# Performance work log

Measured on AMD Instinct MI355X. Metric: run time of the kernel, lower is better.

## Reference

```python
import jax, jax.numpy as jnp
import numpy as np

# irreps = 128x0e + 64x1e + 32x2e  (dim = 128 + 64*3 + 32*5 = 480)
# hidden = 512x0e + 256x1e + 128x2e ; gate scalars = (256+128) x0e
N = 65536
M0, M1, M2 = 128, 64, 32          # input multiplicities per degree l=0,1,2
H0, H1, H2 = 512, 256, 128        # hidden multiplicities
G = H1 + H2                       # number of sigmoid gate scalars
EPS = 1e-8
S0 = float(np.sqrt(M0)); S1 = float(np.sqrt(M1)); S2 = float(np.sqrt(M2))
T0 = float(np.sqrt(H0)); T1 = float(np.sqrt(H1)); T2 = float(np.sqrt(H2))


def setup_inputs() -> dict:
    key = jax.random.key(0)
    ks = jax.random.split(key, 8)
    p = lambda k, shape: jax.random.normal(k, shape, dtype=jnp.float32)
    return dict(
        x=p(ks[0], (N, M0 + 3 * M1 + 5 * M2)),
        # SeperableLayerNorm affine params (weight per channel; bias only for scalars)
        nw0=jnp.ones((M0,), jnp.float32), nb0=jnp.zeros((M0,), jnp.float32),
        nw1=jnp.ones((M1,), jnp.float32), nw2=jnp.ones((M2,), jnp.float32),
        # lin1: irreps -> (hidden scalars + gates) 0e, hidden 1e, hidden 2e. e3nn fan-in norm.
        W0=p(ks[1], (M0, H0 + G)), b0=jnp.zeros((H0 + G,), jnp.float32),
        W1=p(ks[2], (M1, H1)), W2=p(ks[3], (M2, H2)),
        # lin2: gated hidden -> irreps
        V0=p(ks[4], (H0, M0)), c0=jnp.zeros((M0,), jnp.float32),
        V1=p(ks[5], (H1, M1)), V2=p(ks[6], (H2, M2)),
        alpha=jnp.float32(0.5),
    )


def _ffn(x, nw0, nb0, nw1, nw2, W0, b0, W1, W2, V0, c0, V1, V2, alpha):
    n = x.shape[0]
    x0 = x[:, :M0]                                   # [n, 128] scalars
    x1 = x[:, M0:M0 + 3 * M1].reshape(n, M1, 3)      # [n, 64, 3]
    x2 = x[:, M0 + 3 * M1:].reshape(n, M2, 5)        # [n, 32, 5]

    # --- SeperableLayerNorm (component norm, std_balance_degrees) ---
    # scalars: standard layer norm over scalar channels
    mu = jnp.mean(x0, axis=-1, keepdims=True)
    xc = x0 - mu
    y0 = xc * jax.lax.rsqrt(jnp.mean(xc * xc, axis=-1, keepdims=True) + EPS) * nw0 + nb0
    # l>0: RMS norm, each degree contributes equally (balance over degrees)
    s1 = jnp.mean(x1 * x1, axis=(1, 2))
    s2 = jnp.mean(x2 * x2, axis=(1, 2))
    inv = jax.lax.rsqrt(0.5 * (s1 + s2) + EPS)[:, None, None]
    y1 = x1 * inv * nw1[:, None]
    y2 = x2 * inv * nw2[:, None]

    # --- lin1 (e3nn Linear: per-degree block matmul, 1/sqrt(fan_in), bias on 0e) ---
    h0 = y0 @ W0 / S0 + b0                            # [n, 896]
    h1 = jnp.einsum('num,uw->nwm', y1, W1) / S1       # [n, 256, 3]
    h2 = jnp.einsum('num,uw->nwm', y2, W2) / S2       # [n, 128, 5]

    # --- Gate: silu on hidden scalars, sigmoid gates broadcast onto l>0 ---
    s = jax.nn.silu(h0[:, :H0])
    g = jax.nn.sigmoid(h0[:, H0:])
    z1 = h1 * g[:, :H1, None]
    z2 = h2 * g[:, H1:, None]

    # --- lin2 ---
    o0 = s @ V0 / T0 + c0
    o1 = jnp.einsum('num,uw->nwm', z1, V1) / T1
    o2 = jnp.einsum('num,uw->nwm', z2, V2) / T2
    dx = jnp.concatenate([o0, o1.reshape(n, -1), o2.reshape(n, -1)], axis=-1)
    return x + jnp.tanh(alpha) * dx


def reference(x, nw0, nb0, nw1, nw2, W0, b0, W1, W2, V0, c0, V1, V2, alpha):
    return _ffn(x, nw0, nb0, nw1, nw2, W0, b0, W1, W2, V0, c0, V1, V2, alpha)
```

## Files before the change

kernel.cpp:

```cpp
#include <hip/hip_runtime.h>
#include <stdint.h>

#define NROWS 65536
#define DCOL  480
#define RT    16

#define INV_S0 0.08838834764831845f
#define INV_S1 0.125f
#define INV_S2 0.17677669529663687f
#define INV_T0 0.044194173824159216f
#define INV_T1 0.0625f
#define INV_T2 0.08838834764831845f

#define OFF_W0T 0
#define OFF_W1T 114688
#define OFF_W2T 131072
#define OFF_V0T 135168
#define OFF_V1T 200704
#define OFF_V2T 217088
#define TOT_W   221184

typedef __attribute__((ext_vector_type(8))) short  short8;
typedef __attribute__((ext_vector_type(4))) float  floatx4;

__device__ __forceinline__ uint16_t f2bf(float x){
  uint32_t u = __builtin_bit_cast(uint32_t, x);
  return (uint16_t)((u + 0x8000u) >> 16);
}
__device__ __forceinline__ float bf2f(uint16_t h){
  return __builtin_bit_cast(float, (uint32_t)h << 16);
}

#define MFMA16(a,b,c) __builtin_amdgcn_mfma_f32_16x16x32_bf16((a),(b),(c),0,0,0)

__global__ __launch_bounds__(256)
void convert_weights(const float* __restrict__ W0, const float* __restrict__ W1,
                     const float* __restrict__ W2, const float* __restrict__ V0,
                     const float* __restrict__ V1, const float* __restrict__ V2,
                     uint16_t* __restrict__ wt)
{
  const int tid = blockIdx.x*256 + threadIdx.x;
  if (tid >= TOT_W) return;
  if (tid < OFF_W1T){
    const int i = tid;            const int n = i>>7, k = i&127;
    wt[tid] = f2bf(W0[(size_t)k*896 + n] * INV_S0);
  } else if (tid < OFF_W2T){
    const int i = tid - OFF_W1T;  const int n = i>>6, k = i&63;
    wt[tid] = f2bf(W1[(size_t)k*256 + n] * INV_S1);
  } else if (tid < OFF_V0T){
    const int i = tid - OFF_W2T;  const int n = i>>5, k = i&31;
    wt[tid] = f2bf(W2[(size_t)k*128 + n] * INV_S2);
  } else if (tid < OFF_V1T){
    const int i = tid - OFF_V0T;  const int n = i>>9, k = i&511;
    wt[tid] = f2bf(V0[(size_t)k*128 + n] * INV_T0);
  } else if (tid < OFF_V2T){
    const int i = tid - OFF_V1T;  const int n = i>>8, k = i&255;
    wt[tid] = f2bf(V1[(size_t)k*64 + n] * INV_T1);
  } else {
    const int i = tid - OFF_V2T;  const int n = i>>7, k = i&127;
    wt[tid] = f2bf(V2[(size_t)k*32 + n] * INV_T2);
  }
}

__global__ __launch_bounds__(256, 3)
void ffn_mfma(const float* __restrict__ x,  const float* __restrict__ nw0,
              const float* __restrict__ nb0,const float* __restrict__ nw1,
              const float* __restrict__ nw2,const float* __restrict__ b0,
              const float* __restrict__ c0, const float* __restrict__ alpha,
              const uint16_t* __restrict__ wt, float* __restrict__ out)
{
  __shared__ __align__(16) uint16_t y0bf[16][136];
  __shared__ __align__(16) uint16_t y1bf[3][16][72];
  __shared__ __align__(16) uint16_t y2bf[5][16][40];
  __shared__ __align__(16) uint16_t gbf[16][392];
  __shared__ __align__(16) uint16_t sbf[16][520];

  const int t      = threadIdx.x;
  const int wave   = t >> 6, lane = t & 63;
  const int lane16 = lane & 15, quad = lane >> 4;
  const int row0   = blockIdx.x * RT;
  const float ta   = tanhf(alpha[0]);

  {
    for (int rr = 0; rr < 4; ++rr){
      const int r = wave*4 + rr;
      const float* xr = x + (size_t)(row0 + r)*DCOL;
      float xv[8];
      #pragma unroll
      for (int i=0;i<8;++i){ const int e = lane + i*64; xv[i] = (e < DCOL) ? xr[e] : 0.f; }
      float s0  = xv[0] + xv[1];
      float s0q = xv[0]*xv[0] + xv[1]*xv[1];
      float q1  = xv[2]*xv[2] + xv[3]*xv[3] + xv[4]*xv[4];
      float q2  = xv[5]*xv[5] + xv[6]*xv[6] + xv[7]*xv[7];
      #pragma unroll
      for (int off=32; off>0; off>>=1){
        s0  += __shfl_xor(s0,  off);
        s0q += __shfl_xor(s0q, off);
        q1  += __shfl_xor(q1,  off);
        q2  += __shfl_xor(q2,  off);
      }
      const float mu   = s0 * (1.f/128.f);
      const float var  = s0q * (1.f/128.f) - mu*mu;
      const float rstd = rsqrtf(var + 1e-8f);
      const float inv  = rsqrtf(0.5f*(q1*(1.f/192.f) + q2*(1.f/160.f)) + 1e-8f);
      #pragma unroll
      for (int i=0;i<8;++i){
        const int e = lane + i*64;
        if (e < 128){
          y0bf[r][e] = f2bf((xv[i]-mu)*rstd*nw0[e] + nb0[e]);
        } else if (e < 320){
          const int d = e - 128; const int u = d/3, mm = d - 3*u;
          y1bf[mm][r][u] = f2bf(xv[i]*inv*nw1[u]);
        } else if (e < DCOL){
          const int d = e - 320; const int u = d/5, mm = d - 5*u;
          y2bf[mm][r][u] = f2bf(xv[i]*inv*nw2[u]);
        }
      }
    }
  }
  __syncthreads();

  {
    short8 a0[4];
    #pragma unroll
    for (int kk=0; kk<4; ++kk)
      a0[kk] = *(const short8*)&y0bf[lane16][kk*32 + quad*8];
    const uint16_t* W0t = wt + OFF_W0T;
    #pragma unroll 1
    for (int tile = wave; tile < 56; tile += 4){
      const int n0 = tile*16;
      floatx4 acc = {0.f,0.f,0.f,0.f};
      #pragma unroll
      for (int kk=0; kk<4; ++kk){
        const short8 b = *(const short8*)(W0t + (size_t)(n0+lane16)*128 + kk*32 + quad*8);
        acc = MFMA16(a0[kk], b, acc);
      }
      const int col  = n0 + lane16;
      const float bias = b0[col];
      #pragma unroll
      for (int r2=0; r2<4; ++r2){
        const int row = quad*4 + r2;
        const float h  = acc[r2] + bias;
        const float sg = 1.f/(1.f + __expf(-h));
        if (col < 512) sbf[row][col]       = f2bf(h*sg);
        else           gbf[row][col - 512] = f2bf(sg);
      }
    }
  }
  __syncthreads();

  {
    const uint16_t* V0t = wt + OFF_V0T;
    const int n0a = wave*16, n0b = (wave+4)*16;
    floatx4 acc0 = {0.f,0.f,0.f,0.f}, acc1 = {0.f,0.f,0.f,0.f};
    #pragma unroll 2
    for (int kk=0; kk<16; ++kk){
      const short8 a  = *(const short8*)&sbf[lane16][kk*32 + quad*8];
      const short8 ba = *(const short8*)(V0t + (size_t)(n0a+lane16)*512 + kk*32 + quad*8);
      const short8 bb = *(const short8*)(V0t + (size_t)(n0b+lane16)*512 + kk*32 + quad*8);
      acc0 = MFMA16(a, ba, acc0);
      acc1 = MFMA16(a, bb, acc1);
    }
    #pragma unroll
    for (int tt=0; tt<2; ++tt){
      const int col = (tt ? n0b : n0a) + lane16;
      const float cc = c0[col];
      const floatx4 acc = tt ? acc1 : acc0;
      #pragma unroll
      for (int r2=0; r2<4; ++r2){
        const int row = quad*4 + r2;
        const size_t idx = (size_t)(row0+row)*DCOL + col;
        out[idx] = x[idx] + ta*(acc[r2] + cc);
      }
    }
  }
  __syncthreads();

  uint16_t (*zbf1)[264] = (uint16_t (*)[264])&sbf[0][0];
  uint16_t (*zbf2)[136] = (uint16_t (*)[136])&sbf[0][0];

  {
    const uint16_t* W1t = wt + OFF_W1T;
    const uint16_t* V1t = wt + OFF_V1T;
    #pragma unroll 1
    for (int m=0; m<3; ++m){
      {
        const short8 a0 = *(const short8*)&y1bf[m][lane16][quad*8];
        const short8 a1 = *(const short8*)&y1bf[m][lane16][32 + quad*8];
        #pragma unroll 1
        for (int tile = wave; tile < 16; tile += 4){
          const int n0 = tile*16;
          floatx4 acc = {0.f,0.f,0.f,0.f};
          const short8 b0f = *(const short8*)(W1t + (size_t)(n0+lane16)*64 + quad*8);
          const short8 b1f = *(const short8*)(W1t + (size_t)(n0+lane16)*64 + 32 + quad*8);
          acc = MFMA16(a0, b0f, acc);
          acc = MFMA16(a1, b1f, acc);
          const int col = n0 + lane16;
          #pragma unroll
          for (int r2=0; r2<4; ++r2){
            const int row = quad*4 + r2;
            const float g = bf2f(gbf[row][col]);
            zbf1[row][col] = f2bf(acc[r2]*g);
          }
        }
      }
      __syncthreads();
      {
        const int n0 = wave*16;
        floatx4 acc = {0.f,0.f,0.f,0.f};
        #pragma unroll
        for (int kk=0; kk<8; ++kk){
          const short8 a = *(const short8*)&zbf1[lane16][kk*32 + quad*8];
          const short8 b = *(const short8*)(V1t + (size_t)(n0+lane16)*256 + kk*32 + quad*8);
          acc = MFMA16(a, b, acc);
        }
        const int col = n0 + lane16;
        #pragma unroll
        for (int r2=0; r2<4; ++r2){
          const int row = quad*4 + r2;
          const size_t idx = (size_t)(row0+row)*DCOL + 128 + col*3 + m;
          out[idx] = x[idx] + ta*acc[r2];
        }
      }
      __syncthreads();
    }
  }

  {
    const uint16_t* W2t = wt + OFF_W2T;
    const uint16_t* V2t = wt + OFF_V2T;
    #pragma unroll 1
    for (int m=0; m<5; ++m){
      {
        const short8 a0 = *(const short8*)&y2bf[m][lane16][quad*8];
        #pragma unroll 1
        for (int tile = wave; tile < 8; tile += 4){
          const int n0 = tile*16;
          floatx4 acc = {0.f,0.f,0.f,0.f};
          const short8 b = *(const short8*)(W2t + (size_t)(n0+lane16)*32 + quad*8);
          acc = MFMA16(a0, b, acc);
          const int col = n0 + lane16;
          #pragma unroll
          for (int r2=0; r2<4; ++r2){
            const int row = quad*4 + r2;
            const float g = bf2f(gbf[row][256 + col]);
            zbf2[row][col] = f2bf(acc[r2]*g);
          }
        }
      }
      __syncthreads();
      if (wave < 2){
        const int n0 = wave*16;
        floatx4 acc = {0.f,0.f,0.f,0.f};
        #pragma unroll
        for (int kk=0; kk<4; ++kk){
          const short8 a = *(const short8*)&zbf2[lane16][kk*32 + quad*8];
          const short8 b = *(const short8*)(V2t + (size_t)(n0+lane16)*128 + kk*32 + quad*8);
          acc = MFMA16(a, b, acc);
        }
        const int col = n0 + lane16;
        #pragma unroll
        for (int r2=0; r2<4; ++r2){
          const int row = quad*4 + r2;
          const size_t idx = (size_t)(row0+row)*DCOL + 320 + col*5 + m;
          out[idx] = x[idx] + ta*acc[r2];
        }
      }
      __syncthreads();
    }
  }
}

extern "C" void kernel_launch(void* const* d_in, const int* in_sizes, int n_in,
                              void* d_out, int out_size, void* d_ws, size_t ws_size,
                              hipStream_t stream) {
  const float* x   = (const float*)d_in[0];
  const float* nw0 = (const float*)d_in[1];
  const float* nb0 = (const float*)d_in[2];
  const float* nw1 = (const float*)d_in[3];
  const float* nw2 = (const float*)d_in[4];
  const float* W0  = (const float*)d_in[5];
  const float* b0  = (const float*)d_in[6];
  const float* W1  = (const float*)d_in[7];
  const float* W2  = (const float*)d_in[8];
  const float* V0  = (const float*)d_in[9];
  const float* c0  = (const float*)d_in[10];
  const float* V1  = (const float*)d_in[11];
  const float* V2  = (const float*)d_in[12];
  const float* al  = (const float*)d_in[13];
  uint16_t* wt = (uint16_t*)d_ws;

  convert_weights<<<dim3((TOT_W + 255)/256), dim3(256), 0, stream>>>(
      W0, W1, W2, V0, V1, V2, wt);
  ffn_mfma<<<dim3(NROWS/RT), dim3(256), 0, stream>>>(
      x, nw0, nb0, nw1, nw2, b0, c0, al, wt, (float*)d_out);
}
```

Baseline: 516.9 us.

## Software-pipeline stage schedule, interleave l=1/l=2 gate stages, cut barriers

Result: faster. 471.4 us (-8.8%).

```diff
diff --git a/kernel.cpp b/kernel.cpp
--- a/kernel.cpp
+++ b/kernel.cpp
@@ -69,29 +69,50 @@
               const float* __restrict__ c0, const float* __restrict__ alpha,
               const uint16_t* __restrict__ wt, float* __restrict__ out)
 {
-  __shared__ __align__(16) uint16_t y0bf[16][136];
   __shared__ __align__(16) uint16_t y1bf[3][16][72];
   __shared__ __align__(16) uint16_t y2bf[5][16][40];
   __shared__ __align__(16) uint16_t gbf[16][392];
-  __shared__ __align__(16) uint16_t sbf[16][520];
+  __shared__ __align__(16) uint16_t Ubuf[12800];
+
+  uint16_t (*y0bf)[136] = (uint16_t (*)[136])(Ubuf);
+  uint16_t (*sbf )[520] = (uint16_t (*)[520])(Ubuf + 2176);
+  uint16_t (*z1b0)[264] = (uint16_t (*)[264])(Ubuf + 2176);
+  uint16_t (*z1b1)[264] = (uint16_t (*)[264])(Ubuf + 6400);
+  uint16_t (*z2b0)[136] = (uint16_t (*)[136])(Ubuf + 10624);
+  uint16_t (*z2b1)[136] = (uint16_t (*)[136])(Ubuf);
 
   const int t      = threadIdx.x;
   const int wave   = t >> 6, lane = t & 63;
   const int lane16 = lane & 15, quad = lane >> 4;
   const int row0   = blockIdx.x * RT;
   const float ta   = tanhf(alpha[0]);
-
-  {
-    for (int rr = 0; rr < 4; ++rr){
-      const int r = wave*4 + rr;
-      const float* xr = x + (size_t)(row0 + r)*DCOL;
-      float xv[8];
-      #pragma unroll
-      for (int i=0;i<8;++i){ const int e = lane + i*64; xv[i] = (e < DCOL) ? xr[e] : 0.f; }
-      float s0  = xv[0] + xv[1];
-      float s0q = xv[0]*xv[0] + xv[1]*xv[1];
-      float q1  = xv[2]*xv[2] + xv[3]*xv[3] + xv[4]*xv[4];
-      float q2  = xv[5]*xv[5] + xv[6]*xv[6] + xv[7]*xv[7];
+  const floatx4 fz = {0.f,0.f,0.f,0.f};
+
+  {
+    float xv[4][8];
+    const int rbase = wave*4;
+    #pragma unroll
+    for (int rr=0; rr<4; ++rr){
+      const float* xr = x + (size_t)(row0 + rbase + rr)*DCOL;
+      #pragma unroll
+      for (int i=0;i<8;++i){ const int e = lane + i*64; xv[rr][i] = (e < DCOL) ? xr[e] : 0.f; }
+    }
+    float wA[8], wB[8]; int uu[8], mmv[8];
+    #pragma unroll
+    for (int i=0;i<8;++i){
+      const int e = lane + i*64;
+      if (e < 128){ uu[i]=e; mmv[i]=0; wA[i]=nw0[e]; wB[i]=nb0[e]; }
+      else if (e < 320){ const int d=e-128; const int u=d/3; uu[i]=u; mmv[i]=d-3*u; wA[i]=nw1[u]; wB[i]=0.f; }
+      else if (e < DCOL){ const int d=e-320; const int u=d/5; uu[i]=u; mmv[i]=d-5*u; wA[i]=nw2[u]; wB[i]=0.f; }
+      else { uu[i]=0; mmv[i]=0; wA[i]=0.f; wB[i]=0.f; }
+    }
+    #pragma unroll
+    for (int rr=0; rr<4; ++rr){
+      const int r = rbase + rr;
+      float s0  = xv[rr][0] + xv[rr][1];
+      float s0q = xv[rr][0]*xv[rr][0] + xv[rr][1]*xv[rr][1];
+      float q1  = xv[rr][2]*xv[rr][2] + xv[rr][3]*xv[rr][3] + xv[rr][4]*xv[rr][4];
+      float q2  = xv[rr][5]*xv[rr][5] + xv[rr][6]*xv[rr][6] + xv[rr][7]*xv[rr][7];
       #pragma unroll
       for (int off=32; off>0; off>>=1){
         s0  += __shfl_xor(s0,  off);
@@ -106,15 +127,9 @@
       #pragma unroll
       for (int i=0;i<8;++i){
         const int e = lane + i*64;
-        if (e < 128){
-          y0bf[r][e] = f2bf((xv[i]-mu)*rstd*nw0[e] + nb0[e]);
-        } else if (e < 320){
-          const int d = e - 128; const int u = d/3, mm = d - 3*u;
-          y1bf[mm][r][u] = f2bf(xv[i]*inv*nw1[u]);
-        } else if (e < DCOL){
-          const int d = e - 320; const int u = d/5, mm = d - 5*u;
-          y2bf[mm][r][u] = f2bf(xv[i]*inv*nw2[u]);
-        }
+        if (e < 128)       y0bf[r][e] = f2bf((xv[rr][i]-mu)*rstd*wA[i] + wB[i]);
+        else if (e < 320)  y1bf[mmv[i]][r][uu[i]] = f2bf(xv[rr][i]*inv*wA[i]);
+        else if (e < DCOL) y2bf[mmv[i]][r][uu[i]] = f2bf(xv[rr][i]*inv*wA[i]);
       }
     }
   }
@@ -126,16 +141,17 @@
     for (int kk=0; kk<4; ++kk)
       a0[kk] = *(const short8*)&y0bf[lane16][kk*32 + quad*8];
     const uint16_t* W0t = wt + OFF_W0T;
-    #pragma unroll 1
-    for (int tile = wave; tile < 56; tile += 4){
-      const int n0 = tile*16;
-      floatx4 acc = {0.f,0.f,0.f,0.f};
-      #pragma unroll
-      for (int kk=0; kk<4; ++kk){
-        const short8 b = *(const short8*)(W0t + (size_t)(n0+lane16)*128 + kk*32 + quad*8);
-        acc = MFMA16(a0[kk], b, acc);
-      }
-      const int col  = n0 + lane16;
+
+    auto ldW0 = [&](int tile, short8* dst){
+      #pragma unroll
+      for (int kk=0;kk<4;++kk)
+        dst[kk] = *(const short8*)(W0t + (size_t)(tile*16+lane16)*128 + kk*32 + quad*8);
+    };
+    auto h0_tile = [&](int tile, const short8* bfr){
+      floatx4 acc = fz;
+      #pragma unroll
+      for (int kk=0;kk<4;++kk) acc = MFMA16(a0[kk], bfr[kk], acc);
+      const int col  = tile*16 + lane16;
       const float bias = b0[col];
       #pragma unroll
       for (int r2=0; r2<4; ++r2){
@@ -145,15 +161,37 @@
         if (col < 512) sbf[row][col]       = f2bf(h*sg);
         else           gbf[row][col - 512] = f2bf(sg);
       }
-    }
-  }
-  __syncthreads();
-
-  {
+    };
+
+    short8 bA[4], bB[4];
+    ldW0(wave, bA);
+    #pragma unroll 1
+    for (int it=0; it<7; ++it){
+      const int tA = wave + it*8, tB = tA + 4;
+      ldW0(tB, bB);
+      h0_tile(tA, bA);
+      if (it < 6) ldW0(tA + 8, bA);
+      h0_tile(tB, bB);
+    }
+  }
+  __syncthreads();
+
+  {
+    const uint16_t* W2t = wt + OFF_W2T;
     const uint16_t* V0t = wt + OFF_V0T;
     const int n0a = wave*16, n0b = (wave+4)*16;
-    floatx4 acc0 = {0.f,0.f,0.f,0.f}, acc1 = {0.f,0.f,0.f,0.f};
-    #pragma unroll 2
+    const short8 a2  = *(const short8*)&y2bf[0][lane16][quad*8];
+    const short8 hba = *(const short8*)(W2t + (size_t)(n0a+lane16)*32 + quad*8);
+    const short8 hbb = *(const short8*)(W2t + (size_t)(n0b+lane16)*32 + quad*8);
+    float xra[4], xrb[4];
+    #pragma unroll
+    for (int r2=0;r2<4;++r2){
+      const int row = quad*4+r2;
+      xra[r2] = x[(size_t)(row0+row)*DCOL + n0a + lane16];
+      xrb[r2] = x[(size_t)(row0+row)*DCOL + n0b + lane16];
+    }
+    floatx4 acc0 = fz, acc1 = fz;
+    #pragma unroll 4
     for (int kk=0; kk<16; ++kk){
       const short8 a  = *(const short8*)&sbf[lane16][kk*32 + quad*8];
       const short8 ba = *(const short8*)(V0t + (size_t)(n0a+lane16)*512 + kk*32 + quad*8);
@@ -161,112 +199,322 @@
       acc0 = MFMA16(a, ba, acc0);
       acc1 = MFMA16(a, bb, acc1);
     }
-    #pragma unroll
-    for (int tt=0; tt<2; ++tt){
-      const int col = (tt ? n0b : n0a) + lane16;
-      const float cc = c0[col];
-      const floatx4 acc = tt ? acc1 : acc0;
-      #pragma unroll
-      for (int r2=0; r2<4; ++r2){
-        const int row = quad*4 + r2;
-        const size_t idx = (size_t)(row0+row)*DCOL + col;
-        out[idx] = x[idx] + ta*(acc[r2] + cc);
-      }
-    }
-  }
-  __syncthreads();
-
-  uint16_t (*zbf1)[264] = (uint16_t (*)[264])&sbf[0][0];
-  uint16_t (*zbf2)[136] = (uint16_t (*)[136])&sbf[0][0];
+    {
+      floatx4 ha = MFMA16(a2, hba, fz);
+      floatx4 hb = MFMA16(a2, hbb, fz);
+      #pragma unroll
+      for (int r2=0;r2<4;++r2){
+        const int row = quad*4+r2;
+        const int ca = n0a+lane16, cb = n0b+lane16;
+        z2b0[row][ca] = f2bf(ha[r2]*bf2f(gbf[row][256+ca]));
+        z2b0[row][cb] = f2bf(hb[r2]*bf2f(gbf[row][256+cb]));
+      }
+    }
+    const float cca = c0[n0a+lane16], ccb = c0[n0b+lane16];
+    #pragma unroll
+    for (int r2=0;r2<4;++r2){
+      const int row = quad*4+r2;
+      out[(size_t)(row0+row)*DCOL + n0a+lane16] = xra[r2] + ta*(acc0[r2]+cca);
+      out[(size_t)(row0+row)*DCOL + n0b+lane16] = xrb[r2] + ta*(acc1[r2]+ccb);
+    }
+  }
+  __syncthreads();
 
   {
     const uint16_t* W1t = wt + OFF_W1T;
-    const uint16_t* V1t = wt + OFF_V1T;
-    #pragma unroll 1
-    for (int m=0; m<3; ++m){
-      {
-        const short8 a0 = *(const short8*)&y1bf[m][lane16][quad*8];
-        const short8 a1 = *(const short8*)&y1bf[m][lane16][32 + quad*8];
-        #pragma unroll 1
-        for (int tile = wave; tile < 16; tile += 4){
-          const int n0 = tile*16;
-          floatx4 acc = {0.f,0.f,0.f,0.f};
-          const short8 b0f = *(const short8*)(W1t + (size_t)(n0+lane16)*64 + quad*8);
-          const short8 b1f = *(const short8*)(W1t + (size_t)(n0+lane16)*64 + 32 + quad*8);
-          acc = MFMA16(a0, b0f, acc);
-          acc = MFMA16(a1, b1f, acc);
-          const int col = n0 + lane16;
-          #pragma unroll
-          for (int r2=0; r2<4; ++r2){
-            const int row = quad*4 + r2;
-            const float g = bf2f(gbf[row][col]);
-            zbf1[row][col] = f2bf(acc[r2]*g);
-          }
-        }
-      }
-      __syncthreads();
-      {
-        const int n0 = wave*16;
-        floatx4 acc = {0.f,0.f,0.f,0.f};
-        #pragma unroll
-        for (int kk=0; kk<8; ++kk){
-          const short8 a = *(const short8*)&zbf1[lane16][kk*32 + quad*8];
-          const short8 b = *(const short8*)(V1t + (size_t)(n0+lane16)*256 + kk*32 + quad*8);
-          acc = MFMA16(a, b, acc);
-        }
-        const int col = n0 + lane16;
-        #pragma unroll
-        for (int r2=0; r2<4; ++r2){
-          const int row = quad*4 + r2;
-          const size_t idx = (size_t)(row0+row)*DCOL + 128 + col*3 + m;
-          out[idx] = x[idx] + ta*acc[r2];
-        }
-      }
-      __syncthreads();
-    }
-  }
-
-  {
     const uint16_t* W2t = wt + OFF_W2T;
     const uint16_t* V2t = wt + OFF_V2T;
-    #pragma unroll 1
-    for (int m=0; m<5; ++m){
-      {
-        const short8 a0 = *(const short8*)&y2bf[m][lane16][quad*8];
-        #pragma unroll 1
-        for (int tile = wave; tile < 8; tile += 4){
-          const int n0 = tile*16;
-          floatx4 acc = {0.f,0.f,0.f,0.f};
-          const short8 b = *(const short8*)(W2t + (size_t)(n0+lane16)*32 + quad*8);
-          acc = MFMA16(a0, b, acc);
-          const int col = n0 + lane16;
-          #pragma unroll
-          for (int r2=0; r2<4; ++r2){
-            const int row = quad*4 + r2;
-            const float g = bf2f(gbf[row][256 + col]);
-            zbf2[row][col] = f2bf(acc[r2]*g);
-          }
-        }
-      }
-      __syncthreads();
-      if (wave < 2){
-        const int n0 = wave*16;
-        floatx4 acc = {0.f,0.f,0.f,0.f};
-        #pragma unroll
-        for (int kk=0; kk<4; ++kk){
-          const short8 a = *(const short8*)&zbf2[lane16][kk*32 + quad*8];
-          const short8 b = *(const short8*)(V2t + (size_t)(n0+lane16)*128 + kk*32 + quad*8);
-          acc = MFMA16(a, b, acc);
-        }
-        const int col = n0 + lane16;
-        #pragma unroll
-        for (int r2=0; r2<4; ++r2){
-          const int row = quad*4 + r2;
-          const size_t idx = (size_t)(row0+row)*DCOL + 320 + col*5 + m;
-          out[idx] = x[idx] + ta*acc[r2];
-        }
-      }
-      __syncthreads();
+    const int n0a = wave*16, n0b = (wave+4)*16;
+    const short8 a2  = *(const short8*)&y2bf[1][lane16][quad*8];
+    const short8 hba = *(const short8*)(W2t + (size_t)(n0a+lane16)*32 + quad*8);
+    const short8 hbb = *(const short8*)(W2t + (size_t)(n0b+lane16)*32 + quad*8);
+    short8 ob[4]; float xro[4];
+    if (wave < 2){
+      const int n0 = wave*16;
+      #pragma unroll
+      for (int kk=0;kk<4;++kk)
+        ob[kk] = *(const short8*)(V2t + (size_t)(n0+lane16)*128 + kk*32 + quad*8);
+      #pragma unroll
+      for (int r2=0;r2<4;++r2)
+        xro[r2] = x[(size_t)(row0+quad*4+r2)*DCOL + 320 + (n0+lane16)*5 + 0];
+    }
+    short8 a10[2], a11[2];
+    a10[0] = *(const short8*)&y1bf[0][lane16][quad*8];
+    a10[1] = *(const short8*)&y1bf[0][lane16][32 + quad*8];
+    a11[0] = *(const short8*)&y1bf[1][lane16][quad*8];
+    a11[1] = *(const short8*)&y1bf[1][lane16][32 + quad*8];
+    #pragma unroll
+    for (int t4=0; t4<4; ++t4){
+      const int n0 = (wave + t4*4)*16;
+      const short8 b0f = *(const short8*)(W1t + (size_t)(n0+lane16)*64 + quad*8);
+      const short8 b1f = *(const short8*)(W1t + (size_t)(n0+lane16)*64 + 32 + quad*8);
+      floatx4 am0 = fz, am1 = fz;
+      am0 = MFMA16(a10[0], b0f, am0); am0 = MFMA16(a10[1], b1f, am0);
+      am1 = MFMA16(a11[0], b0f, am1); am1 = MFMA16(a11[1], b1f, am1);
+      const int col = n0 + lane16;
+      #pragma unroll
+      for (int r2=0;r2<4;++r2){
+        const int row = quad*4 + r2;
+        const float g = bf2f(gbf[row][col]);
+        z1b0[row][col] = f2bf(am0[r2]*g);
+        z1b1[row][col] = f2bf(am1[r2]*g);
+      }
+    }
+    {
+      floatx4 ha = MFMA16(a2, hba, fz);
+      floatx4 hb = MFMA16(a2, hbb, fz);
+      #pragma unroll
+      for (int r2=0;r2<4;++r2){
+        const int row = quad*4+r2;
+        const int ca = n0a+lane16, cb = n0b+lane16;
+        z2b1[row][ca] = f2bf(ha[r2]*bf2f(gbf[row][256+ca]));
+        z2b1[row][cb] = f2bf(hb[r2]*bf2f(gbf[row][256+cb]));
+      }
+    }
+    if (wave < 2){
+      const int n0 = wave*16;
+      floatx4 acc = fz;
+      #pragma unroll
+      for (int kk=0;kk<4;++kk){
+        const short8 a = *(const short8*)&z2b0[lane16][kk*32 + quad*8];
+        acc = MFMA16(a, ob[kk], acc);
+      }
+      const int col = n0 + lane16;
+      #pragma unroll
+      for (int r2=0;r2<4;++r2){
+        const int row = quad*4+r2;
+        const size_t idx = (size_t)(row0+row)*DCOL + 320 + col*5 + 0;
+        out[idx] = xro[r2] + ta*acc[r2];
+      }
+    }
+  }
+  __syncthreads();
+
+  {
+    const uint16_t* V1t = wt + OFF_V1T;
+    const uint16_t* W2t = wt + OFF_W2T;
+    const uint16_t* V2t = wt + OFF_V2T;
+    const int n0a = wave*16, n0b = (wave+4)*16;
+    const short8 a2  = *(const short8*)&y2bf[2][lane16][quad*8];
+    const short8 hba = *(const short8*)(W2t + (size_t)(n0a+lane16)*32 + quad*8);
+    const short8 hbb = *(const short8*)(W2t + (size_t)(n0b+lane16)*32 + quad*8);
+    short8 ob[4]; float xro[4];
+    if (wave >= 2){
+      const int n0 = (wave-2)*16;
+      #pragma unroll
+      for (int kk=0;kk<4;++kk)
+        ob[kk] = *(const short8*)(V2t + (size_t)(n0+lane16)*128 + kk*32 + quad*8);
+      #pragma unroll
+      for (int r2=0;r2<4;++r2)
+        xro[r2] = x[(size_t)(row0+quad*4+r2)*DCOL + 320 + (n0+lane16)*5 + 1];
+    }
+    const int n0 = wave*16;
+    float xr0[4], xr1[4];
+    #pragma unroll
+    for (int r2=0;r2<4;++r2){
+      const int row = quad*4+r2;
+      xr0[r2] = x[(size_t)(row0+row)*DCOL + 128 + (n0+lane16)*3 + 0];
+      xr1[r2] = x[(size_t)(row0+row)*DCOL + 128 + (n0+lane16)*3 + 1];
+    }
+    floatx4 am0 = fz, am1 = fz;
+    #pragma unroll 4
+    for (int kk=0; kk<8; ++kk){
+      const short8 af0 = *(const short8*)&z1b0[lane16][kk*32 + quad*8];
+      const short8 af1 = *(const short8*)&z1b1[lane16][kk*32 + quad*8];
+      const short8 b   = *(const short8*)(V1t + (size_t)(n0+lane16)*256 + kk*32 + quad*8);
+      am0 = MFMA16(af0, b, am0);
+      am1 = MFMA16(af1, b, am1);
+    }
+    const int col = n0 + lane16;
+    #pragma unroll
+    for (int r2=0;r2<4;++r2){
+      const int row = quad*4+r2;
+      out[(size_t)(row0+row)*DCOL + 128 + col*3 + 0] = xr0[r2] + ta*am0[r2];
+      out[(size_t)(row0+row)*DCOL + 128 + col*3 + 1] = xr1[r2] + ta*am1[r2];
+    }
+    {
+      floatx4 ha = MFMA16(a2, hba, fz);
+      floatx4 hb = MFMA16(a2, hbb, fz);
+      #pragma unroll
+      for (int r2=0;r2<4;++r2){
+        const int row = quad*4+r2;
+        const int ca = n0a+lane16, cb = n0b+lane16;
+        z2b0[row][ca] = f2bf(ha[r2]*bf2f(gbf[row][256+ca]));
+        z2b0[row][cb] = f2bf(hb[r2]*bf2f(gbf[row][256+cb]));
+      }
+    }
+    if (wave >= 2){
+      const int n02 = (wave-2)*16;
+      floatx4 acc = fz;
+      #pragma unroll
+      for (int kk=0;kk<4;++kk){
+        const short8 a = *(const short8*)&z2b1[lane16][kk*32 + quad*8];
+        acc = MFMA16(a, ob[kk], acc);
+      }
+      const int c2 = n02 + lane16;
+      #pragma unroll
+      for (int r2=0;r2<4;++r2){
+        const int row = quad*4+r2;
+        const size_t idx = (size_t)(row0+row)*DCOL + 320 + c2*5 + 1;
+        out[idx] = xro[r2] + ta*acc[r2];
+      }
+    }
+  }
+  __syncthreads();
+
+  {
+    const uint16_t* W1t = wt + OFF_W1T;
+    const uint16_t* W2t = wt + OFF_W2T;
+    const uint16_t* V2t = wt + OFF_V2T;
+    const int n0a = wave*16, n0b = (wave+4)*16;
+    const short8 a2  = *(const short8*)&y2bf[3][lane16][quad*8];
+    const short8 hba = *(const short8*)(W2t + (size_t)(n0a+lane16)*32 + quad*8);
+    const short8 hbb = *(const short8*)(W2t + (size_t)(n0b+lane16)*32 + quad*8);
+    short8 ob[4]; float xro[4];
+    if (wave < 2){
+      const int n0 = wave*16;
+      #pragma unroll
+      for (int kk=0;kk<4;++kk)
+        ob[kk] = *(const short8*)(V2t + (size_t)(n0+lane16)*128 + kk*32 + quad*8);
+      #pragma unroll
+      for (int r2=0;r2<4;++r2)
+        xro[r2] = x[(size_t)(row0+quad*4+r2)*DCOL + 320 + (n0+lane16)*5 + 2];
+    }
+    short8 a12[2];
+    a12[0] = *(const short8*)&y1bf[2][lane16][quad*8];
+    a12[1] = *(const short8*)&y1bf[2][lane16][32 + quad*8];
+    #pragma unroll
+    for (int t4=0; t4<4; ++t4){
+      const int n0 = (wave + t4*4)*16;
+      const short8 b0f = *(const short8*)(W1t + (size_t)(n0+lane16)*64 + quad*8);
+      const short8 b1f = *(const short8*)(W1t + (size_t)(n0+lane16)*64 + 32 + quad*8);
+      floatx4 am = fz;
+      am = MFMA16(a12[0], b0f, am); am = MFMA16(a12[1], b1f, am);
+      const int col = n0 + lane16;
+      #pragma unroll
+      for (int r2=0;r2<4;++r2){
+        const int row = quad*4 + r2;
+        z1b0[row][col] = f2bf(am[r2]*bf2f(gbf[row][col]));
+      }
+    }
+    {
+      floatx4 ha = MFMA16(a2, hba, fz);
+      floatx4 hb = MFMA16(a2, hbb, fz);
+      #pragma unroll
+      for (int r2=0;r2<4;++r2){
+        const int row = quad*4+r2;
+        const int ca = n0a+lane16, cb = n0b+lane16;
+        z2b1[row][ca] = f2bf(ha[r2]*bf2f(gbf[row][256+ca]));
+        z2b1[row][cb] = f2bf(hb[r2]*bf2f(gbf[row][256+cb]));
+      }
+    }
+    if (wave < 2){
+      const int n0 = wave*16;
+      floatx4 acc = fz;
+      #pragma unroll
+      for (int kk=0;kk<4;++kk){
+        const short8 a = *(const short8*)&z2b0[lane16][kk*32 + quad*8];
+        acc = MFMA16(a, ob[kk], acc);
+      }
+      const int col = n0 + lane16;
+      #pragma unroll
+      for (int r2=0;r2<4;++r2){
+        const int row = quad*4+r2;
+        const size_t idx = (size_t)(row0+row)*DCOL + 320 + col*5 + 2;
+        out[idx] = xro[r2] + ta*acc[r2];
+      }
+    }
+  }
+  __syncthreads();
+
+  {
+    const uint16_t* V1t = wt + OFF_V1T;
+    const uint16_t* W2t = wt + OFF_W2T;
+    const uint16_t* V2t = wt + OFF_V2T;
+    const int n0a = wave*16, n0b = (wave+4)*16;
+    const short8 a2  = *(const short8*)&y2bf[4][lane16][quad*8];
+    const short8 hba = *(const short8*)(W2t + (size_t)(n0a+lane16)*32 + quad*8);
+    const short8 hbb = *(const short8*)(W2t + (size_t)(n0b+lane16)*32 + quad*8);
+    short8 ob[4]; float xro[4];
+    if (wave >= 2){
+      const int n0 = (wave-2)*16;
+      #pragma unroll
+      for (int kk=0;kk<4;++kk)
+        ob[kk] = *(const short8*)(V2t + (size_t)(n0+lane16)*128 + kk*32 + quad*8);
+      #pragma unroll
+      for (int r2=0;r2<4;++r2)
+        xro[r2] = x[(size_t)(row0+quad*4+r2)*DCOL + 320 + (n0+lane16)*5 + 3];
+    }
+    const int n0 = wave*16;
+    float xr2[4];
+    #pragma unroll
+    for (int r2=0;r2<4;++r2)
+      xr2[r2] = x[(size_t)(row0+quad*4+r2)*DCOL + 128 + (n0+lane16)*3 + 2];
+    floatx4 am = fz;
+    #pragma unroll 4
+    for (int kk=0; kk<8; ++kk){
+      const short8 a = *(const short8*)&z1b0[lane16][kk*32 + quad*8];
+      const short8 b = *(const short8*)(V1t + (size_t)(n0+lane16)*256 + kk*32 + quad*8);
+      am = MFMA16(a, b, am);
+    }
+    const int col = n0 + lane16;
+    #pragma unroll
+    for (int r2=0;r2<4;++r2){
+      const int row = quad*4+r2;
+      out[(size_t)(row0+row)*DCOL + 128 + col*3 + 2] = xr2[r2] + ta*am[r2];
+    }
+    {
+      floatx4 ha = MFMA16(a2, hba, fz);
+      floatx4 hb = MFMA16(a2, hbb, fz);
+      #pragma unroll
+      for (int r2=0;r2<4;++r2){
+        const int row = quad*4+r2;
+        const int ca = n0a+lane16, cb = n0b+lane16;
+        z2b0[row][ca] = f2bf(ha[r2]*bf2f(gbf[row][256+ca]));
+        z2b0[row][cb] = f2bf(hb[r2]*bf2f(gbf[row][256+cb]));
+      }
+    }
+    if (wave >= 2){
+      const int n02 = (wave-2)*16;
+      floatx4 acc = fz;
+      #pragma unroll
+      for (int kk=0;kk<4;++kk){
+        const short8 a = *(const short8*)&z2b1[lane16][kk*32 + quad*8];
+        acc = MFMA16(a, ob[kk], acc);
+      }
+      const int c2 = n02 + lane16;
+      #pragma unroll
+      for (int r2=0;r2<4;++r2){
+        const int row = quad*4+r2;
+        const size_t idx = (size_t)(row0+row)*DCOL + 320 + c2*5 + 3;
+        out[idx] = xro[r2] + ta*acc[r2];
+      }
+    }
+  }
+  __syncthreads();
+
+  if (wave < 2){
+    const uint16_t* V2t = wt + OFF_V2T;
+    const int n0 = wave*16;
+    short8 ob[4]; float xro[4];
+    #pragma unroll
+    for (int kk=0;kk<4;++kk)
+      ob[kk] = *(const short8*)(V2t + (size_t)(n0+lane16)*128 + kk*32 + quad*8);
+    #pragma unroll
+    for (int r2=0;r2<4;++r2)
+      xro[r2] = x[(size_t)(row0+quad*4+r2)*DCOL + 320 + (n0+lane16)*5 + 4];
+    floatx4 acc = fz;
+    #pragma unroll
+    for (int kk=0;kk<4;++kk){
+      const short8 a = *(const short8*)&z2b0[lane16][kk*32 + quad*8];
+      acc = MFMA16(a, ob[kk], acc);
+    }
+    const int col = n0 + lane16;
+    #pragma unroll
+    for (int r2=0;r2<4;++r2){
+      const int row = quad*4+r2;
+      const size_t idx = (size_t)(row0+row)*DCOL + 320 + col*5 + 4;
+      out[idx] = xro[r2] + ta*acc[r2];
     }
   }
 }
```

## Restructure FFN kernel into 8-wave phases with fewer barriers and an aliased LDS pool

Applied to the files above, without the earlier changes.

New measurement: 429.9 us. 16.8% less time.

```diff
diff --git a/kernel.cpp b/kernel.cpp
--- a/kernel.cpp
+++ b/kernel.cpp
@@ -62,36 +62,55 @@
   }
 }
 
-__global__ __launch_bounds__(256, 3)
+__global__ __launch_bounds__(512, 4)
 void ffn_mfma(const float* __restrict__ x,  const float* __restrict__ nw0,
               const float* __restrict__ nb0,const float* __restrict__ nw1,
               const float* __restrict__ nw2,const float* __restrict__ b0,
               const float* __restrict__ c0, const float* __restrict__ alpha,
               const uint16_t* __restrict__ wt, float* __restrict__ out)
 {
-  __shared__ __align__(16) uint16_t y0bf[16][136];
-  __shared__ __align__(16) uint16_t y1bf[3][16][72];
-  __shared__ __align__(16) uint16_t y2bf[5][16][40];
-  __shared__ __align__(16) uint16_t gbf[16][392];
-  __shared__ __align__(16) uint16_t sbf[16][520];
+  __shared__ __align__(16) uint16_t pool[34304];
+
+  uint16_t (*gbf )[392]      = (uint16_t (*)[392])     (pool);
+  uint16_t (*y1bf)[16][72]   = (uint16_t (*)[16][72])  (pool + 6272);
+  uint16_t (*z2bf)[16][136]  = (uint16_t (*)[16][136]) (pool + 9728);
+  uint16_t (*z1bf)[16][264]  = (uint16_t (*)[16][264]) (pool + 20608);
+  uint16_t (*y2bf)[16][40]   = (uint16_t (*)[16][40])  (pool + 20608);
+  uint16_t (*sbf )[520]      = (uint16_t (*)[520])     (pool + 23808);
+  uint16_t (*y0bf)[136]      = (uint16_t (*)[136])     (pool + 32128);
 
   const int t      = threadIdx.x;
   const int wave   = t >> 6, lane = t & 63;
   const int lane16 = lane & 15, quad = lane >> 4;
   const int row0   = blockIdx.x * RT;
   const float ta   = tanhf(alpha[0]);
-
-  {
-    for (int rr = 0; rr < 4; ++rr){
-      const int r = wave*4 + rr;
-      const float* xr = x + (size_t)(row0 + r)*DCOL;
-      float xv[8];
-      #pragma unroll
-      for (int i=0;i<8;++i){ const int e = lane + i*64; xv[i] = (e < DCOL) ? xr[e] : 0.f; }
-      float s0  = xv[0] + xv[1];
-      float s0q = xv[0]*xv[0] + xv[1]*xv[1];
-      float q1  = xv[2]*xv[2] + xv[3]*xv[3] + xv[4]*xv[4];
-      float q2  = xv[5]*xv[5] + xv[6]*xv[6] + xv[7]*xv[7];
+  const floatx4 fz = {0.f,0.f,0.f,0.f};
+
+  {
+    float xv[2][8];
+    const int rbase = wave*2;
+    #pragma unroll
+    for (int rr=0; rr<2; ++rr){
+      const float* xr = x + (size_t)(row0 + rbase + rr)*DCOL;
+      #pragma unroll
+      for (int i=0;i<8;++i){ const int e = lane + i*64; xv[rr][i] = (e < DCOL) ? xr[e] : 0.f; }
+    }
+    float wA[8], wB[8]; int uu[8], mmv[8];
+    #pragma unroll
+    for (int i=0;i<8;++i){
+      const int e = lane + i*64;
+      if (e < 128){ uu[i]=e; mmv[i]=0; wA[i]=nw0[e]; wB[i]=nb0[e]; }
+      else if (e < 320){ const int d=e-128; const int u=d/3; uu[i]=u; mmv[i]=d-3*u; wA[i]=nw1[u]; wB[i]=0.f; }
+      else if (e < DCOL){ const int d=e-320; const int u=d/5; uu[i]=u; mmv[i]=d-5*u; wA[i]=nw2[u]; wB[i]=0.f; }
+      else { uu[i]=0; mmv[i]=0; wA[i]=0.f; wB[i]=0.f; }
+    }
+    #pragma unroll
+    for (int rr=0; rr<2; ++rr){
+      const int r = rbase + rr;
+      float s0  = xv[rr][0] + xv[rr][1];
+      float s0q = xv[rr][0]*xv[rr][0] + xv[rr][1]*xv[rr][1];
+      float q1  = xv[rr][2]*xv[rr][2] + xv[rr][3]*xv[rr][3] + xv[rr][4]*xv[rr][4];
+      float q2  = xv[rr][5]*xv[rr][5] + xv[rr][6]*xv[rr][6] + xv[rr][7]*xv[rr][7];
       #pragma unroll
       for (int off=32; off>0; off>>=1){
         s0  += __shfl_xor(s0,  off);
@@ -106,15 +125,9 @@
       #pragma unroll
       for (int i=0;i<8;++i){
         const int e = lane + i*64;
-        if (e < 128){
-          y0bf[r][e] = f2bf((xv[i]-mu)*rstd*nw0[e] + nb0[e]);
-        } else if (e < 320){
-          const int d = e - 128; const int u = d/3, mm = d - 3*u;
-          y1bf[mm][r][u] = f2bf(xv[i]*inv*nw1[u]);
-        } else if (e < DCOL){
-          const int d = e - 320; const int u = d/5, mm = d - 5*u;
-          y2bf[mm][r][u] = f2bf(xv[i]*inv*nw2[u]);
-        }
+        if (e < 128)       y0bf[r][e] = f2bf((xv[rr][i]-mu)*rstd*wA[i] + wB[i]);
+        else if (e < 320)  y1bf[mmv[i]][r][uu[i]] = f2bf(xv[rr][i]*inv*wA[i]);
+        else if (e < DCOL) y2bf[mmv[i]][r][uu[i]] = f2bf(xv[rr][i]*inv*wA[i]);
       }
     }
   }
@@ -126,16 +139,17 @@
     for (int kk=0; kk<4; ++kk)
       a0[kk] = *(const short8*)&y0bf[lane16][kk*32 + quad*8];
     const uint16_t* W0t = wt + OFF_W0T;
-    #pragma unroll 1
-    for (int tile = wave; tile < 56; tile += 4){
-      const int n0 = tile*16;
-      floatx4 acc = {0.f,0.f,0.f,0.f};
-      #pragma unroll
-      for (int kk=0; kk<4; ++kk){
-        const short8 b = *(const short8*)(W0t + (size_t)(n0+lane16)*128 + kk*32 + quad*8);
-        acc = MFMA16(a0[kk], b, acc);
-      }
-      const int col  = n0 + lane16;
+
+    auto ldW0 = [&](int tile, short8* dst){
+      #pragma unroll
+      for (int kk=0;kk<4;++kk)
+        dst[kk] = *(const short8*)(W0t + (size_t)(tile*16+lane16)*128 + kk*32 + quad*8);
+    };
+    auto h0_tile = [&](int tile, const short8* bfr){
+      floatx4 acc = fz;
+      #pragma unroll
+      for (int kk=0;kk<4;++kk) acc = MFMA16(a0[kk], bfr[kk], acc);
+      const int col  = tile*16 + lane16;
       const float bias = b0[col];
       #pragma unroll
       for (int r2=0; r2<4; ++r2){
@@ -145,128 +159,159 @@
         if (col < 512) sbf[row][col]       = f2bf(h*sg);
         else           gbf[row][col - 512] = f2bf(sg);
       }
+    };
+
+    short8 buf[2][4];
+    ldW0(wave, buf[0]);
+    #pragma unroll
+    for (int it=0; it<7; ++it){
+      const int cur = it & 1;
+      if (it < 6) ldW0(wave + (it+1)*8, buf[cur^1]);
+      h0_tile(wave + it*8, buf[cur]);
     }
   }
   __syncthreads();
 
   {
+    const uint16_t* W2t = wt + OFF_W2T;
     const uint16_t* V0t = wt + OFF_V0T;
-    const int n0a = wave*16, n0b = (wave+4)*16;
-    floatx4 acc0 = {0.f,0.f,0.f,0.f}, acc1 = {0.f,0.f,0.f,0.f};
-    #pragma unroll 2
+    const int col = wave*16 + lane16;
+    const short8 b2 = *(const short8*)(W2t + (size_t)col*32 + quad*8);
+    short8 a2[5];
+    #pragma unroll
+    for (int m=0;m<5;++m) a2[m] = *(const short8*)&y2bf[m][lane16][quad*8];
+    float g2v[4], xra[4];
+    #pragma unroll
+    for (int r2=0;r2<4;++r2){
+      g2v[r2] = bf2f(gbf[quad*4+r2][256+col]);
+      xra[r2] = x[(size_t)(row0+quad*4+r2)*DCOL + col];
+    }
+    const float cc = c0[col];
+    floatx4 acc = fz;
+    #pragma unroll 4
     for (int kk=0; kk<16; ++kk){
-      const short8 a  = *(const short8*)&sbf[lane16][kk*32 + quad*8];
-      const short8 ba = *(const short8*)(V0t + (size_t)(n0a+lane16)*512 + kk*32 + quad*8);
-      const short8 bb = *(const short8*)(V0t + (size_t)(n0b+lane16)*512 + kk*32 + quad*8);
-      acc0 = MFMA16(a, ba, acc0);
-      acc1 = MFMA16(a, bb, acc1);
-    }
-    #pragma unroll
-    for (int tt=0; tt<2; ++tt){
-      const int col = (tt ? n0b : n0a) + lane16;
-      const float cc = c0[col];
-      const floatx4 acc = tt ? acc1 : acc0;
-      #pragma unroll
-      for (int r2=0; r2<4; ++r2){
-        const int row = quad*4 + r2;
-        const size_t idx = (size_t)(row0+row)*DCOL + col;
-        out[idx] = x[idx] + ta*(acc[r2] + cc);
-      }
-    }
+      const short8 a = *(const short8*)&sbf[lane16][kk*32 + quad*8];
+      const short8 b = *(const short8*)(V0t + (size_t)col*512 + kk*32 + quad*8);
+      acc = MFMA16(a, b, acc);
+    }
+    #pragma unroll
+    for (int m=0;m<5;++m){
+      floatx4 h = MFMA16(a2[m], b2, fz);
+      #pragma unroll
+      for (int r2=0;r2<4;++r2)
+        z2bf[m][quad*4+r2][col] = f2bf(h[r2]*g2v[r2]);
+    }
+    #pragma unroll
+    for (int r2=0;r2<4;++r2)
+      out[(size_t)(row0+quad*4+r2)*DCOL + col] = xra[r2] + ta*(acc[r2]+cc);
   }
   __syncthreads();
 
-  uint16_t (*zbf1)[264] = (uint16_t (*)[264])&sbf[0][0];
-  uint16_t (*zbf2)[136] = (uint16_t (*)[136])&sbf[0][0];
-
-  {
-    const uint16_t* W1t = wt + OFF_W1T;
+  {
+    if (wave < 6){
+      const uint16_t* W1t = wt + OFF_W1T;
+      short8 a1[3][2];
+      #pragma unroll
+      for (int m=0;m<3;++m){
+        a1[m][0] = *(const short8*)&y1bf[m][lane16][quad*8];
+        a1[m][1] = *(const short8*)&y1bf[m][lane16][32 + quad*8];
+      }
+      const int nt    = (wave < 4) ? 3 : 2;
+      const int tbase = (wave < 4) ? wave*3 : 12 + (wave-4)*2;
+      #pragma unroll 1
+      for (int tt=0; tt<nt; ++tt){
+        const int col = (tbase+tt)*16 + lane16;
+        const short8 b0f = *(const short8*)(W1t + (size_t)col*64 + quad*8);
+        const short8 b1f = *(const short8*)(W1t + (size_t)col*64 + 32 + quad*8);
+        float gv[4];
+        #pragma unroll
+        for (int r2=0;r2<4;++r2) gv[r2] = bf2f(gbf[quad*4+r2][col]);
+        #pragma unroll
+        for (int m=0;m<3;++m){
+          floatx4 am = MFMA16(a1[m][0], b0f, fz);
+          am = MFMA16(a1[m][1], b1f, am);
+          #pragma unroll
+          for (int r2=0;r2<4;++r2)
+            z1bf[m][quad*4+r2][col] = f2bf(am[r2]*gv[r2]);
+        }
+      }
+    } else {
+      const uint16_t* V2t = wt + OFF_V2T;
+      const int col = (wave-6)*16 + lane16;
+      short8 ob[4];
+      #pragma unroll
+      for (int kk=0;kk<4;++kk)
+        ob[kk] = *(const short8*)(V2t + (size_t)col*128 + kk*32 + quad*8);
+      float xo[5][4];
+      #pragma unroll
+      for (int m=0;m<5;++m)
+        #pragma unroll
+        for (int r2=0;r2<4;++r2)
+          xo[m][r2] = x[(size_t)(row0+quad*4+r2)*DCOL + 320 + col*5 + m];
+      floatx4 am[5];
+      #pragma unroll
+      for (int m=0;m<5;++m){
+        am[m] = fz;
+        #pragma unroll
+        for (int kk=0;kk<4;++kk){
+          const short8 a = *(const short8*)&z2bf[m][lane16][kk*32 + quad*8];
+          am[m] = MFMA16(a, ob[kk], am[m]);
+        }
+      }
+      #pragma unroll
+      for (int m=0;m<5;++m)
+        #pragma unroll
+        for (int r2=0;r2<4;++r2){
+          const size_t idx = (size_t)(row0+quad*4+r2)*DCOL + 320 + col*5 + m;
+          out[idx] = xo[m][r2] + ta*am[m][r2];
+        }
+    }
+  }
+  __syncthreads();
+
+  {
     const uint16_t* V1t = wt + OFF_V1T;
-    #pragma unroll 1
-    for (int m=0; m<3; ++m){
-      {
-        const short8 a0 = *(const short8*)&y1bf[m][lane16][quad*8];
-        const short8 a1 = *(const short8*)&y1bf[m][lane16][32 + quad*8];
-        #pragma unroll 1
-        for (int tile = wave; tile < 16; tile += 4){
-          const int n0 = tile*16;
-          floatx4 acc = {0.f,0.f,0.f,0.f};
-          const short8 b0f = *(const short8*)(W1t + (size_t)(n0+lane16)*64 + quad*8);
-          const short8 b1f = *(const short8*)(W1t + (size_t)(n0+lane16)*64 + 32 + quad*8);
-          acc = MFMA16(a0, b0f, acc);
-          acc = MFMA16(a1, b1f, acc);
-          const int col = n0 + lane16;
-          #pragma unroll
-          for (int r2=0; r2<4; ++r2){
-            const int row = quad*4 + r2;
-            const float g = bf2f(gbf[row][col]);
-            zbf1[row][col] = f2bf(acc[r2]*g);
-          }
-        }
-      }
-      __syncthreads();
-      {
-        const int n0 = wave*16;
-        floatx4 acc = {0.f,0.f,0.f,0.f};
-        #pragma unroll
-        for (int kk=0; kk<8; ++kk){
-          const short8 a = *(const short8*)&zbf1[lane16][kk*32 + quad*8];
-          const short8 b = *(const short8*)(V1t + (size_t)(n0+lane16)*256 + kk*32 + quad*8);
-          acc = MFMA16(a, b, acc);
-        }
-        const int col = n0 + lane16;
-        #pragma unroll
-        for (int r2=0; r2<4; ++r2){
-          const int row = quad*4 + r2;
-          const size_t idx = (size_t)(row0+row)*DCOL + 128 + col*3 + m;
-          out[idx] = x[idx] + ta*acc[r2];
-        }
-      }
-      __syncthreads();
-    }
-  }
-
-  {
-    const uint16_t* W2t = wt + OFF_W2T;
-    const uint16_t* V2t = wt + OFF_V2T;
-    #pragma unroll 1
-    for (int m=0; m<5; ++m){
-      {
-        const short8 a0 = *(const short8*)&y2bf[m][lane16][quad*8];
-        #pragma unroll 1
-        for (int tile = wave; tile < 8; tile += 4){
-          const int n0 = tile*16;
-          floatx4 acc = {0.f,0.f,0.f,0.f};
-          const short8 b = *(const short8*)(W2t + (size_t)(n0+lane16)*32 + quad*8);
-          acc = MFMA16(a0, b, acc);
-          const int col = n0 + lane16;
-          #pragma unroll
-          for (int r2=0; r2<4; ++r2){
-            const int row = quad*4 + r2;
-            const float g = bf2f(gbf[row][256 + col]);
-            zbf2[row][col] = f2bf(acc[r2]*g);
-          }
-        }
-      }
-      __syncthreads();
-      if (wave < 2){
-        const int n0 = wave*16;
-        floatx4 acc = {0.f,0.f,0.f,0.f};
-        #pragma unroll
-        for (int kk=0; kk<4; ++kk){
-          const short8 a = *(const short8*)&zbf2[lane16][kk*32 + quad*8];
-          const short8 b = *(const short8*)(V2t + (size_t)(n0+lane16)*128 + kk*32 + quad*8);
-          acc = MFMA16(a, b, acc);
-        }
-        const int col = n0 + lane16;
-        #pragma unroll
-        for (int r2=0; r2<4; ++r2){
-          const int row = quad*4 + r2;
-          const size_t idx = (size_t)(row0+row)*DCOL + 320 + col*5 + m;
-          out[idx] = x[idx] + ta*acc[r2];
-        }
-      }
-      __syncthreads();
+    const int col = (wave & 3)*16 + lane16;
+    short8 vb[8];
+    #pragma unroll
+    for (int kk=0;kk<8;++kk)
+      vb[kk] = *(const short8*)(V1t + (size_t)col*256 + kk*32 + quad*8);
+    if (wave < 4){
+      float xr0[4], xr2[4];
+      #pragma unroll
+      for (int r2=0;r2<4;++r2){
+        const size_t base = (size_t)(row0+quad*4+r2)*DCOL + 128 + col*3;
+        xr0[r2] = x[base + 0];
+        xr2[r2] = x[base + 2];
+      }
+      floatx4 am0 = fz, am2 = fz;
+      #pragma unroll
+      for (int kk=0;kk<8;++kk){
+        const short8 f0 = *(const short8*)&z1bf[0][lane16][kk*32 + quad*8];
+        const short8 f2 = *(const short8*)&z1bf[2][lane16][kk*32 + quad*8];
+        am0 = MFMA16(f0, vb[kk], am0);
+        am2 = MFMA16(f2, vb[kk], am2);
+      }
+      #pragma unroll
+      for (int r2=0;r2<4;++r2){
+        const size_t base = (size_t)(row0+quad*4+r2)*DCOL + 128 + col*3;
+        out[base + 0] = xr0[r2] + ta*am0[r2];
+        out[base + 2] = xr2[r2] + ta*am2[r2];
+      }
+    } else {
+      float xr1[4];
+      #pragma unroll
+      for (int r2=0;r2<4;++r2)
+        xr1[r2] = x[(size_t)(row0+quad*4+r2)*DCOL + 128 + col*3 + 1];
+      floatx4 am1 = fz;
+      #pragma unroll
+      for (int kk=0;kk<8;++kk){
+        const short8 f1 = *(const short8*)&z1bf[1][lane16][kk*32 + quad*8];
+        am1 = MFMA16(f1, vb[kk], am1);
+      }
+      #pragma unroll
+      for (int r2=0;r2<4;++r2)
+        out[(size_t)(row0+quad*4+r2)*DCOL + 128 + col*3 + 1] = xr1[r2] + ta*am1[r2];
     }
   }
 }
@@ -292,6 +337,6 @@
 
   convert_weights<<<dim3((TOT_W + 255)/256), dim3(256), 0, stream>>>(
       W0, W1, W2, V0, V1, V2, wt);
-  ffn_mfma<<<dim3(NROWS/RT), dim3(256), 0, stream>>>(
+  ffn_mfma<<<dim3(NROWS/RT), dim3(512), 0, stream>>>(
       x, nw0, nb0, nw1, nw2, b0, c0, al, wt, (float*)d_out);
 }
```
